# Optimization experiments

Measured on AMD Instinct MI355X. Metric: run time of the kernel, lower is better.

The kernel has to match this reference:

```python
import jax, jax.numpy as jnp
import numpy as np

N = 100000      # nodes
E = 1600000     # edges (before self-loops)
F_IN = 128      # num_features
C = 32          # embedding_dim / output_dim per head
H = 4           # heads
SLOPE = 0.2     # PyG GATv2Conv default negative_slope


def setup_inputs() -> dict:
    key = jax.random.key(0)
    ks = jax.random.split(key, 16)
    def w(k, shp, fan):
        return jax.random.normal(k, shp, jnp.float32) / np.float32(np.sqrt(fan))
    return {
        "x": jax.random.normal(ks[0], (N, F_IN), jnp.float32),
        "edge_index": jax.random.randint(ks[1], (2, E), 0, N, jnp.int32),
        "W1l": w(ks[2], (F_IN, H * C), F_IN),
        "W1r": w(ks[3], (F_IN, H * C), F_IN),
        "att1": w(ks[4], (H, C), C),
        "b1": jnp.zeros((H * C,), jnp.float32),
        "W2l": w(ks[5], (H * C, H * C), H * C),
        "W2r": w(ks[6], (H * C, H * C), H * C),
        "att2": w(ks[7], (H, C), C),
        "b2": jnp.zeros((H * C,), jnp.float32),
        "W3l": w(ks[8], (H * C, H * C), H * C),
        "W3r": w(ks[9], (H * C, H * C), H * C),
        "att3": w(ks[10], (H, C), C),
        "b3": jnp.zeros((C,), jnp.float32),
    }


def gatv2_conv(x, src, dst, Wl, Wr, att, b, concat):
    """GATv2Conv: gather -> LeakyReLU attention -> segment softmax -> scatter-add."""
    n = x.shape[0]
    h, c = att.shape
    xl = (x @ Wl).reshape(n, h, c)   # source-side projection
    xr = (x @ Wr).reshape(n, h, c)   # target-side projection
    e = jax.nn.leaky_relu(xl[src] + xr[dst], SLOPE)          # [E, H, C]
    logits = jnp.einsum('ehc,hc->eh', e, att)                # [E, H]
    m = jax.ops.segment_max(logits, dst, num_segments=n)     # per-dst max
    ex = jnp.exp(logits - m[dst])
    den = jax.ops.segment_sum(ex, dst, num_segments=n)
    alpha = ex / den[dst]                                    # [E, H]
    out = jax.ops.segment_sum(alpha[:, :, None] * xl[src], dst, num_segments=n)  # [N,H,C]
    out = out.reshape(n, h * c) if concat else out.mean(axis=1)
    return out + b


def reference(x, edge_index, W1l, W1r, att1, b1, W2l, W2r, att2, b2, W3l, W3r, att3, b3):
    n = x.shape[0]
    loops = jnp.arange(n, dtype=edge_index.dtype)            # PyG adds self-loops
    src = jnp.concatenate([edge_index[0], loops])
    dst = jnp.concatenate([edge_index[1], loops])
    h = jax.nn.relu(gatv2_conv(x, src, dst, W1l, W1r, att1, b1, True))
    h = jax.nn.relu(gatv2_conv(h, src, dst, W2l, W2r, att2, b2, True))
    h = jax.nn.relu(gatv2_conv(h, src, dst, W3l, W3r, att3, b3, False))
    return h
```

## Files before the change

### kernel.cpp

```cpp
#include <hip/hip_runtime.h>
#include <hip/hip_bf16.h>
#include <hip/hip_fp16.h>

#define SLOPE 0.2f

typedef __attribute__((ext_vector_type(8))) short bf16x8;
typedef __attribute__((ext_vector_type(4))) float f32x4;

__device__ __forceinline__ unsigned short bf16_rn(float f) {
    unsigned u = __float_as_uint(f);
    return (unsigned short)((u + 0x7FFFu + ((u >> 16) & 1u)) >> 16);
}
__device__ __forceinline__ float bf16_to_f32(unsigned short s) {
    return __uint_as_float(((unsigned)s) << 16);
}


__global__ __launch_bounds__(256) void fat_prep(const float* __restrict__ W0, const float* __restrict__ W1,
                                                const float* __restrict__ W2, const float* __restrict__ W3,
                                                const float* __restrict__ W4, const float* __restrict__ W5,
                                                unsigned short* __restrict__ Wtab,
                                                const int* __restrict__ dstv, int* __restrict__ deg, int E) {
    int b = blockIdx.x, t = threadIdx.x;
    if (b < 384) {
        int j = b >> 6;
        int e = ((b & 63) << 8) + t;
        const float* W = (j == 0) ? W0 : (j == 1) ? W1 : (j == 2) ? W2
                       : (j == 3) ? W3 : (j == 4) ? W4 : W5;
        int L = j >> 1, side = j & 1;
        unsigned short* hiT = Wtab + (size_t)L * 65536 + side * 16384;
        unsigned short* loT = hiT + 32768;
        int n = e >> 7, k = e & 127;
        float x = W[k * 128 + n];
        unsigned short h = bf16_rn(x);
        hiT[e] = h;
        loT[e] = bf16_rn(x - bf16_to_f32(h));
    } else {
        int i = (b - 384) * 256 + t;
        if (i < E) atomicAdd(&deg[dstv[i]], 1);
    }
}


__global__ __launch_bounds__(256) void k_scan(const int* __restrict__ in, int* __restrict__ out,
                                              int* bsums, int n) {
    __shared__ int wsum[4];
    int t = threadIdx.x;
    int base = blockIdx.x * 1024 + t * 4;
    int v0 = (base + 0 < n) ? in[base + 0] : 0;
    int v1 = (base + 1 < n) ? in[base + 1] : 0;
    int v2 = (base + 2 < n) ? in[base + 2] : 0;
    int v3 = (base + 3 < n) ? in[base + 3] : 0;
    int tsum = v0 + v1 + v2 + v3;
    int lane = t & 63, wid = t >> 6;
    int x = tsum;
    #pragma unroll
    for (int d = 1; d < 64; d <<= 1) {
        int y = __shfl_up(x, d);
        if (lane >= d) x += y;
    }
    if (lane == 63) wsum[wid] = x;
    __syncthreads();
    if (t == 0) {
        int a = 0;
        for (int w = 0; w < 4; ++w) { int b = wsum[w]; wsum[w] = a; a += b; }
    }
    __syncthreads();
    int excl = x - tsum + wsum[wid];
    if (base + 0 < n) out[base + 0] = excl;
    if (base + 1 < n) out[base + 1] = excl + v0;
    if (base + 2 < n) out[base + 2] = excl + v0 + v1;
    if (base + 3 < n) out[base + 3] = excl + v0 + v1 + v2;
    if (bsums != nullptr && t == 255) bsums[blockIdx.x] = excl + tsum;
}

__global__ __launch_bounds__(256) void k_scan_add(const int* __restrict__ dscan,
                                                  const int* __restrict__ boff,
                                                  int* __restrict__ rowptr, int* __restrict__ cursor,
                                                  int n, int total) {
    int i = blockIdx.x * 256 + threadIdx.x;
    if (i < n) {
        int v = dscan[i] + boff[i >> 10];
        rowptr[i] = v;
        cursor[i] = v;
    }
    if (i == n) rowptr[n] = total;
}


#define LDS_A_HI 0
#define LDS_A_LO 10240
#define LDS_B_HI 20480
#define LDS_B_LO 30720

__device__ __forceinline__ void gemm_block(const float* __restrict__ X,
                                           const unsigned short* __restrict__ WL,
                                           __half* __restrict__ Y0, float* __restrict__ Y1,
                                           int M, int tile, int ysel,
                                           unsigned char* lds, int t) {
    const unsigned short* whi = WL + ysel * 16384;
    const unsigned short* wlo = whi + 32768;
    int row0 = tile * 128;
    int lane = t & 63, w = t >> 6;
    int ml = lane & 15, q = lane >> 4;
    int sm = t >> 1, sh = t & 1;
    int srow = row0 + sm;
    bool svalid = srow < M;

    f32x4 acc[2][8];
    #pragma unroll
    for (int i = 0; i < 2; ++i)
        #pragma unroll
        for (int j = 0; j < 8; ++j) acc[i][j] = (f32x4){0.f, 0.f, 0.f, 0.f};

    for (int ks = 0; ks < 4; ++ks) {
        int k0 = ks * 32;
        {
            float v[16];
            if (svalid) {
                const float* src = X + (size_t)srow * 128 + k0 + sh * 16;
                *(float4*)&v[0]  = *(const float4*)&src[0];
                *(float4*)&v[4]  = *(const float4*)&src[4];
                *(float4*)&v[8]  = *(const float4*)&src[8];
                *(float4*)&v[12] = *(const float4*)&src[12];
            } else {
                #pragma unroll
                for (int j = 0; j < 16; ++j) v[j] = 0.f;
            }
            unsigned hw[8], lw[8];
            #pragma unroll
            for (int j = 0; j < 8; ++j) {
                unsigned short h0 = bf16_rn(v[2 * j]);
                unsigned short h1 = bf16_rn(v[2 * j + 1]);
                unsigned short l0 = bf16_rn(v[2 * j] - bf16_to_f32(h0));
                unsigned short l1 = bf16_rn(v[2 * j + 1] - bf16_to_f32(h1));
                hw[j] = (unsigned)h0 | ((unsigned)h1 << 16);
                lw[j] = (unsigned)l0 | ((unsigned)l1 << 16);
            }
            unsigned char* pa = lds + LDS_A_HI + sm * 80 + sh * 32;
            *(uint4*)(pa)      = *(uint4*)&hw[0];
            *(uint4*)(pa + 16) = *(uint4*)&hw[4];
            unsigned char* pl = lds + LDS_A_LO + sm * 80 + sh * 32;
            *(uint4*)(pl)      = *(uint4*)&lw[0];
            *(uint4*)(pl + 16) = *(uint4*)&lw[4];
        }
        {
            #pragma unroll
            for (int cc = 0; cc < 2; ++cc) {
                int c = t + cc * 256;
                int n = c >> 2, kc = (c & 3) * 8;
                *(uint4*)(lds + LDS_B_HI + n * 80 + (c & 3) * 16) =
                    *(const uint4*)(whi + n * 128 + k0 + kc);
                *(uint4*)(lds + LDS_B_LO + n * 80 + (c & 3) * 16) =
                    *(const uint4*)(wlo + n * 128 + k0 + kc);
            }
        }
        __syncthreads();
        bf16x8 ah[2], al[2];
        #pragma unroll
        for (int mt = 0; mt < 2; ++mt) {
            int am = w * 32 + mt * 16 + ml;
            ah[mt] = *(const bf16x8*)(lds + LDS_A_HI + am * 80 + q * 16);
            al[mt] = *(const bf16x8*)(lds + LDS_A_LO + am * 80 + q * 16);
        }
        #pragma unroll
        for (int nt = 0; nt < 8; ++nt) {
            int bn = nt * 16 + ml;
            bf16x8 bh = *(const bf16x8*)(lds + LDS_B_HI + bn * 80 + q * 16);
            bf16x8 bl = *(const bf16x8*)(lds + LDS_B_LO + bn * 80 + q * 16);
            #pragma unroll
            for (int mt = 0; mt < 2; ++mt) {
                acc[mt][nt] = __builtin_amdgcn_mfma_f32_16x16x32_bf16(ah[mt], bh, acc[mt][nt], 0, 0, 0);
                acc[mt][nt] = __builtin_amdgcn_mfma_f32_16x16x32_bf16(ah[mt], bl, acc[mt][nt], 0, 0, 0);
                acc[mt][nt] = __builtin_amdgcn_mfma_f32_16x16x32_bf16(al[mt], bh, acc[mt][nt], 0, 0, 0);
            }
        }
        __syncthreads();
    }

    if (ysel == 0) {
        #pragma unroll
        for (int mt = 0; mt < 2; ++mt) {
            int rbase = row0 + w * 32 + mt * 16 + q * 4;
            #pragma unroll
            for (int r = 0; r < 4; ++r) {
                int row = rbase + r;
                if (row < M) {
                    #pragma unroll
                    for (int nt = 0; nt < 8; ++nt)
                        Y0[(size_t)row * 128 + nt * 16 + ml] = __float2half(acc[mt][nt][r]);
                }
            }
        }
    } else {
        #pragma unroll
        for (int mt = 0; mt < 2; ++mt) {
            int rbase = row0 + w * 32 + mt * 16 + q * 4;
            #pragma unroll
            for (int r = 0; r < 4; ++r) {
                int row = rbase + r;
                if (row < M) {
                    #pragma unroll
                    for (int nt = 0; nt < 8; ++nt)
                        Y1[(size_t)row * 128 + nt * 16 + ml] = acc[mt][nt][r];
                }
            }
        }
    }
}

__global__ __launch_bounds__(256) void k_gemm(const float* __restrict__ X,
                                              const unsigned short* __restrict__ WL,
                                              __half* __restrict__ Y0, float* __restrict__ Y1, int M) {
    __shared__ __align__(16) unsigned char lds[40960];
    gemm_block(X, WL, Y0, Y1, M, blockIdx.x, blockIdx.y, lds, threadIdx.x);
}


__global__ __launch_bounds__(256) void fat_g1(const float* __restrict__ X,
                                              const unsigned short* __restrict__ WL,
                                              __half* __restrict__ Y0, float* __restrict__ Y1, int M,
                                              const int* __restrict__ srcv, const int* __restrict__ dstv,
                                              int* __restrict__ cursor, int* __restrict__ col, int E) {
    __shared__ __align__(16) unsigned char lds[40960];
    int tiles = (M + 127) >> 7;
    int tid = blockIdx.x * 256 + threadIdx.x;
    int T = gridDim.x * 256;

    int ps[4], ss[4];
    #pragma unroll
    for (int i = 0; i < 4; ++i) {
        int idx = tid + i * T;
        if (idx < E) {
            ss[i] = srcv[idx];
            ps[i] = atomicAdd(&cursor[dstv[idx]], 1);
        } else {
            ps[i] = -1;
        }
    }

    gemm_block(X, WL, Y0, Y1, M, blockIdx.x % tiles, blockIdx.x / tiles, lds, threadIdx.x);

    #pragma unroll
    for (int i = 0; i < 4; ++i)
        if (ps[i] >= 0) col[ps[i]] = ss[i];
}


__device__ __forceinline__ float quadsum(float t) {
    t += __int_as_float(__builtin_amdgcn_update_dpp(0, __float_as_int(t), 0xB1, 0xf, 0xf, true));
    t += __int_as_float(__builtin_amdgcn_update_dpp(0, __float_as_int(t), 0x4E, 0xf, 0xf, true));
    return t;
}

template <bool MEAN>
__global__ __launch_bounds__(256) void fused_gat(const __half* __restrict__ XLh,
                                                 const float* __restrict__ XR,
                                                 const float* __restrict__ att,
                                                 const float* __restrict__ bias,
                                                 const int* __restrict__ rowptr,
                                                 const int* __restrict__ col,
                                                 float* __restrict__ OUT, int N) {
    int wave = (blockIdx.x * blockDim.x + threadIdx.x) >> 6;
    int lane = threadIdx.x & 63;
    int g = lane >> 4, sub = lane & 15;
    int dst = wave * 4 + g;
    bool vd = dst < N;
    int d0 = vd ? dst : 0;

    int start = vd ? rowptr[d0] : 0;
    int end   = vd ? rowptr[d0 + 1] : 0;

    float xr[8], av[8];
    {
        const float* xrp = &XR[(size_t)d0 * 128 + sub * 8];
        *(float4*)&xr[0] = *(const float4*)&xrp[0];
        *(float4*)&xr[4] = *(const float4*)&xrp[4];
        *(float4*)&av[0] = *(const float4*)&att[sub * 8];
        *(float4*)&av[4] = *(const float4*)&att[sub * 8 + 4];
    }

    int deg = end - start;
    int md = max(deg, __shfl_xor(deg, 16));
    md = max(md, __shfl_xor(md, 32));

    float acc[8];
    float s;
    {
        uint4 r = *(const uint4*)&XLh[(size_t)d0 * 128 + sub * 8];
        float xs[8];
        const __half2* h = (const __half2*)&r;
        #pragma unroll
        for (int qq = 0; qq < 4; ++qq) {
            float2 f = __half22float2(h[qq]);
            xs[2 * qq] = f.x; xs[2 * qq + 1] = f.y;
        }
        float dS = 0.f;
        #pragma unroll
        for (int j = 0; j < 8; ++j) {
            float u = xs[j] + xr[j];
            u = fmaxf(u, SLOPE * u);
            dS = fmaf(u, av[j], dS);
        }
        float tS = quadsum(dS);
        float wS = __expf(fminf(tS, 80.f));
        s = wS;
        #pragma unroll
        for (int j = 0; j < 8; ++j) acc[j] = wS * xs[j];
    }

    for (int i = 0; i < md; i += 2) {
        int pA = start + i, pB = start + i + 1;
        bool vA = pA < end, vB = pB < end;
        int iA = col[vA ? pA : 0];
        int iB = col[vB ? pB : 0];
        uint4 rA = *(const uint4*)&XLh[(size_t)iA * 128 + sub * 8];
        uint4 rB = *(const uint4*)&XLh[(size_t)iB * 128 + sub * 8];
        float xA[8], xB[8];
        {
            const __half2* hA = (const __half2*)&rA;
            const __half2* hB = (const __half2*)&rB;
            #pragma unroll
            for (int qq = 0; qq < 4; ++qq) {
                float2 fA = __half22float2(hA[qq]);
                float2 fB = __half22float2(hB[qq]);
                xA[2 * qq] = fA.x; xA[2 * qq + 1] = fA.y;
                xB[2 * qq] = fB.x; xB[2 * qq + 1] = fB.y;
            }
        }
        float dA = 0.f, dB = 0.f;
        #pragma unroll
        for (int j = 0; j < 8; ++j) {
            float uA = xA[j] + xr[j];
            float uB = xB[j] + xr[j];
            uA = fmaxf(uA, SLOPE * uA);
            uB = fmaxf(uB, SLOPE * uB);
            dA = fmaf(uA, av[j], dA);
            dB = fmaf(uB, av[j], dB);
        }
        float tA = quadsum(dA);
        float tB = quadsum(dB);
        float wA = __expf(fminf(tA, 80.f));
        float wB = __expf(fminf(tB, 80.f));
        wA = vA ? wA : 0.f;
        wB = vB ? wB : 0.f;
        s += wA + wB;
        #pragma unroll
        for (int j = 0; j < 8; ++j) {
            acc[j] = fmaf(wA, xA[j], acc[j]);
            acc[j] = fmaf(wB, xB[j], acc[j]);
        }
    }

    float rs = 1.0f / s;
    if (MEAN) {
        float o[8];
        #pragma unroll
        for (int j = 0; j < 8; ++j) {
            float v = acc[j] * rs;
            v += __shfl_xor(v, 4);
            v += __shfl_xor(v, 8);
            o[j] = fmaxf(fmaf(v, 0.25f, bias[sub * 8 + j]), 0.f);
        }
        if (vd && sub < 4) {
            *(float4*)&OUT[(size_t)dst * 32 + sub * 8]     = *(float4*)&o[0];
            *(float4*)&OUT[(size_t)dst * 32 + sub * 8 + 4] = *(float4*)&o[4];
        }
    } else {
        float o[8];
        #pragma unroll
        for (int j = 0; j < 8; ++j)
            o[j] = fmaxf(fmaf(acc[j], rs, bias[sub * 8 + j]), 0.f);
        if (vd) {
            *(float4*)&OUT[(size_t)dst * 128 + sub * 8]     = *(float4*)&o[0];
            *(float4*)&OUT[(size_t)dst * 128 + sub * 8 + 4] = *(float4*)&o[4];
        }
    }
}


extern "C" void kernel_launch(void* const* d_in, const int* in_sizes, int n_in,
                              void* d_out, int out_size, void* d_ws, size_t ws_size,
                              hipStream_t stream) {
    const float* x   = (const float*)d_in[0];
    const int*   ei  = (const int*)d_in[1];
    const float* W1l = (const float*)d_in[2];
    const float* W1r = (const float*)d_in[3];
    const float* at1 = (const float*)d_in[4];
    const float* b1  = (const float*)d_in[5];
    const float* W2l = (const float*)d_in[6];
    const float* W2r = (const float*)d_in[7];
    const float* at2 = (const float*)d_in[8];
    const float* b2  = (const float*)d_in[9];
    const float* W3l = (const float*)d_in[10];
    const float* W3r = (const float*)d_in[11];
    const float* at3 = (const float*)d_in[12];
    const float* b3  = (const float*)d_in[13];
    float* out = (float*)d_out;

    int N = in_sizes[0] / 128;
    int E = in_sizes[1] / 2;
    const int* srcv = ei;
    const int* dstv = ei + E;

    char* p = (char*)d_ws;
    auto alloc = [&](size_t bytes) -> void* {
        void* r = (void*)p;
        p += (bytes + 255) & ~(size_t)255;
        return r;
    };
    __half* XLh = (__half*)alloc((size_t)N * 128 * 2);
    float*  XR  = (float*)alloc((size_t)N * 128 * 4);
    float*  H   = (float*)alloc((size_t)N * 128 * 4);
    int* rowptr = (int*)alloc((size_t)(N + 1) * 4);
    int* deg    = (int*)alloc((size_t)N * 4);
    int* dscan  = (int*)alloc((size_t)N * 4);
    int* cursor = (int*)alloc((size_t)N * 4);
    int* bsum   = (int*)alloc(1024 * 4);
    int* boff   = (int*)alloc(1024 * 4);
    int* col    = (int*)alloc((size_t)E * 4);
    unsigned short* Wtab = (unsigned short*)alloc((size_t)6 * 65536 * 2);

    int tiles = (N + 127) / 128;
    int nfb = (N + 15) / 16;
    int eb = (E + 255) / 256;

    hipMemsetAsync(deg, 0, (size_t)N * 4, stream);
    fat_prep<<<384 + eb, 256, 0, stream>>>(W1l, W1r, W2l, W2r, W3l, W3r, Wtab, dstv, deg, E);
    int nb = (N + 1023) / 1024;
    k_scan<<<nb, 256, 0, stream>>>(deg, dscan, bsum, N);
    k_scan<<<1, 256, 0, stream>>>(bsum, boff, nullptr, nb);
    k_scan_add<<<(N + 256) / 256, 256, 0, stream>>>(dscan, boff, rowptr, cursor, N, E);
    fat_g1<<<2 * tiles, 256, 0, stream>>>(x, Wtab, XLh, XR, N, srcv, dstv, cursor, col, E);
    fused_gat<false><<<nfb, 256, 0, stream>>>(XLh, XR, at1, b1, rowptr, col, H, N);
    k_gemm<<<dim3(tiles, 2), 256, 0, stream>>>(H, Wtab + 1 * 65536, XLh, XR, N);
    fused_gat<false><<<nfb, 256, 0, stream>>>(XLh, XR, at2, b2, rowptr, col, H, N);
    k_gemm<<<dim3(tiles, 2), 256, 0, stream>>>(H, Wtab + 2 * 65536, XLh, XR, N);
    fused_gat<true><<<nfb, 256, 0, stream>>>(XLh, XR, at3, b3, rowptr, col, out, N);
}
```

Before: 589.6 us.

## Build CSR via two-pass bucketed binning instead of per-edge global atomics

Replaces the per-edge global atomicAdd on a per-destination cursor, which was fused into the first GEMM, with a two-level binning scheme. Edges are first grouped into 256-destination buckets using LDS counters and one global atomic per bucket per block, producing an int2 staging array. A second kernel scatters each bucket into col using LDS cursors. This trades scattered global atomics for extra 8-byte-per-edge staging traffic and two more launches, and the first GEMM no longer overlaps with CSR construction.

Result: no change. 590.3 us (+0.1%).

```diff
diff --git a/kernel.cpp b/kernel.cpp
--- a/kernel.cpp
+++ b/kernel.cpp
@@ -76,15 +76,69 @@
 
 __global__ __launch_bounds__(256) void k_scan_add(const int* __restrict__ dscan,
                                                   const int* __restrict__ boff,
-                                                  int* __restrict__ rowptr, int* __restrict__ cursor,
+                                                  int* __restrict__ rowptr, int* __restrict__ bcur,
                                                   int n, int total) {
     int i = blockIdx.x * 256 + threadIdx.x;
     if (i < n) {
         int v = dscan[i] + boff[i >> 10];
         rowptr[i] = v;
-        cursor[i] = v;
+        if ((i & 255) == 0) bcur[i >> 8] = v;
     }
     if (i == n) rowptr[n] = total;
+}
+
+
+__global__ __launch_bounds__(256) void k_binA(const int* __restrict__ srcv, const int* __restrict__ dstv,
+                                              int* __restrict__ bcur, int2* __restrict__ edge2,
+                                              int E, int NB) {
+    __shared__ int lcnt[512];
+    __shared__ int lbase[512];
+    int t = threadIdx.x;
+    int base = blockIdx.x * 16384;
+    for (int b = t; b < 512; b += 256) lcnt[b] = 0;
+    __syncthreads();
+    #pragma unroll 4
+    for (int j = 0; j < 64; ++j) {
+        int idx = base + j * 256 + t;
+        if (idx < E) atomicAdd(&lcnt[dstv[idx] >> 8], 1);
+    }
+    __syncthreads();
+    for (int b = t; b < NB; b += 256) {
+        int c = lcnt[b];
+        lbase[b] = c ? atomicAdd(&bcur[b], c) : 0;
+        lcnt[b] = 0;
+    }
+    __syncthreads();
+    #pragma unroll 4
+    for (int j = 0; j < 64; ++j) {
+        int idx = base + j * 256 + t;
+        if (idx < E) {
+            int s = srcv[idx], d = dstv[idx];
+            int bk = d >> 8;
+            int off = atomicAdd(&lcnt[bk], 1);
+            edge2[lbase[bk] + off] = make_int2(s, d);
+        }
+    }
+}
+
+
+__global__ __launch_bounds__(256) void k_binB(const int* __restrict__ rowptr,
+                                              const int2* __restrict__ edge2,
+                                              int* __restrict__ col, int N) {
+    __shared__ int cur[256];
+    int t = threadIdx.x;
+    int dstbase = blockIdx.x << 8;
+    int dd = dstbase + t;
+    cur[t] = (dd < N) ? rowptr[dd] : 0;
+    __syncthreads();
+    int beg = rowptr[dstbase];
+    int hi = dstbase + 256; if (hi > N) hi = N;
+    int endd = rowptr[hi];
+    for (int e = beg + t; e < endd; e += 256) {
+        int2 ed = edge2[e];
+        int pos = atomicAdd(&cur[ed.y & 255], 1);
+        col[pos] = ed.x;
+    }
 }
 
 
@@ -214,36 +268,6 @@
                                               __half* __restrict__ Y0, float* __restrict__ Y1, int M) {
     __shared__ __align__(16) unsigned char lds[40960];
     gemm_block(X, WL, Y0, Y1, M, blockIdx.x, blockIdx.y, lds, threadIdx.x);
-}
-
-
-__global__ __launch_bounds__(256) void fat_g1(const float* __restrict__ X,
-                                              const unsigned short* __restrict__ WL,
-                                              __half* __restrict__ Y0, float* __restrict__ Y1, int M,
-                                              const int* __restrict__ srcv, const int* __restrict__ dstv,
-                                              int* __restrict__ cursor, int* __restrict__ col, int E) {
-    __shared__ __align__(16) unsigned char lds[40960];
-    int tiles = (M + 127) >> 7;
-    int tid = blockIdx.x * 256 + threadIdx.x;
-    int T = gridDim.x * 256;
-
-    int ps[4], ss[4];
-    #pragma unroll
-    for (int i = 0; i < 4; ++i) {
-        int idx = tid + i * T;
-        if (idx < E) {
-            ss[i] = srcv[idx];
-            ps[i] = atomicAdd(&cursor[dstv[idx]], 1);
-        } else {
-            ps[i] = -1;
-        }
-    }
-
-    gemm_block(X, WL, Y0, Y1, M, blockIdx.x % tiles, blockIdx.x / tiles, lds, threadIdx.x);
-
-    #pragma unroll
-    for (int i = 0; i < 4; ++i)
-        if (ps[i] >= 0) col[ps[i]] = ss[i];
 }
 
 
@@ -402,6 +426,7 @@
     int E = in_sizes[1] / 2;
     const int* srcv = ei;
     const int* dstv = ei + E;
+    int NB = (N + 255) >> 8;
 
     char* p = (char*)d_ws;
     auto alloc = [&](size_t bytes) -> void* {
@@ -415,10 +440,11 @@
     int* rowptr = (int*)alloc((size_t)(N + 1) * 4);
     int* deg    = (int*)alloc((size_t)N * 4);
     int* dscan  = (int*)alloc((size_t)N * 4);
-    int* cursor = (int*)alloc((size_t)N * 4);
+    int* bcur   = (int*)alloc((size_t)NB * 4);
     int* bsum   = (int*)alloc(1024 * 4);
     int* boff   = (int*)alloc(1024 * 4);
     int* col    = (int*)alloc((size_t)E * 4);
+    int2* edge2 = (int2*)alloc((size_t)E * 8);
     unsigned short* Wtab = (unsigned short*)alloc((size_t)6 * 65536 * 2);
 
     int tiles = (N + 127) / 128;
@@ -430,8 +456,10 @@
     int nb = (N + 1023) / 1024;
     k_scan<<<nb, 256, 0, stream>>>(deg, dscan, bsum, N);
     k_scan<<<1, 256, 0, stream>>>(bsum, boff, nullptr, nb);
-    k_scan_add<<<(N + 256) / 256, 256, 0, stream>>>(dscan, boff, rowptr, cursor, N, E);
-    fat_g1<<<2 * tiles, 256, 0, stream>>>(x, Wtab, XLh, XR, N, srcv, dstv, cursor, col, E);
+    k_scan_add<<<(N + 256) / 256, 256, 0, stream>>>(dscan, boff, rowptr, bcur, N, E);
+    k_binA<<<(E + 16383) / 16384, 256, 0, stream>>>(srcv, dstv, bcur, edge2, E, NB);
+    k_binB<<<NB, 256, 0, stream>>>(rowptr, edge2, col, N);
+    k_gemm<<<dim3(tiles, 2), 256, 0, stream>>>(x, Wtab, XLh, XR, N);
     fused_gat<false><<<nfb, 256, 0, stream>>>(XLh, XR, at1, b1, rowptr, col, H, N);
     k_gemm<<<dim3(tiles, 2), 256, 0, stream>>>(H, Wtab + 1 * 65536, XLh, XR, N);
     fused_gat<false><<<nfb, 256, 0, stream>>>(XLh, XR, at2, b2, rowptr, col, H, N);
```
